# Kernel tuning notes

Hardware: AMD Instinct MI355X
Metric: run time of the kernel (lower is better)

Reference implementation:

```python
import jax, jax.numpy as jnp
import numpy as np

NH, NKV, HD = 16, 4, 64  # num_heads, num_kv_heads, head_dim
ROPE_BASE = 10000.0


def setup_inputs() -> dict:
    key = jax.random.key(0)
    ks = jax.random.split(key, 5)
    B, S, D = 2, 2048, 1024
    x = jax.random.normal(ks[0], (B, S, D), dtype=jnp.float32)
    # torch Linear layout: [out_features, in_features], xavier-ish scale
    Wq = jax.random.normal(ks[1], (NH * HD, D), dtype=jnp.float32) * 0.02
    Wk = jax.random.normal(ks[2], (NKV * HD, D), dtype=jnp.float32) * 0.02
    Wv = jax.random.normal(ks[3], (NKV * HD, D), dtype=jnp.float32) * 0.02
    Wo = jax.random.normal(ks[4], (D, NH * HD), dtype=jnp.float32) * 0.02
    return {"x": x, "Wq": Wq, "Wk": Wk, "Wv": Wv, "Wo": Wo}


def _rotate_half(t):
    t1, t2 = jnp.split(t, 2, axis=-1)
    return jnp.concatenate([-t2, t1], axis=-1)


def _rope_cos_sin(seq_len, dtype):
    inv_freq = 1.0 / (ROPE_BASE ** (jnp.arange(0, HD, 2, dtype=jnp.float32) / HD))
    freqs = jnp.outer(jnp.arange(seq_len, dtype=jnp.float32), inv_freq)  # [S, HD/2]
    emb = jnp.concatenate([freqs, freqs], axis=-1)                       # [S, HD]
    return jnp.cos(emb).astype(dtype), jnp.sin(emb).astype(dtype)


def reference(x, Wq, Wk, Wv, Wo):
    B, S, D = x.shape
    scale = 1.0 / np.sqrt(HD)
    # projections (torch Linear: y = x @ W.T)
    q = jnp.einsum('bsd,ed->bse', x, Wq).reshape(B, S, NH, HD).transpose(0, 2, 1, 3)
    k = jnp.einsum('bsd,ed->bse', x, Wk).reshape(B, S, NKV, HD).transpose(0, 2, 1, 3)
    v = jnp.einsum('bsd,ed->bse', x, Wv).reshape(B, S, NKV, HD).transpose(0, 2, 1, 3)
    # RoPE
    cos, sin = _rope_cos_sin(S, x.dtype)
    cos = cos[None, None]  # [1,1,S,HD]
    sin = sin[None, None]
    q = q * cos + _rotate_half(q) * sin
    k = k * cos + _rotate_half(k) * sin
    # GQA: repeat kv heads (matches expand+reshape: head h = kvh*rep + r)
    rep = NH // NKV
    k = jnp.repeat(k, rep, axis=1)  # [B,NH,S,HD]
    v = jnp.repeat(v, rep, axis=1)
    # scaled dot-product attention, causal
    scores = jnp.einsum('bhqd,bhkd->bhqk', q, k) * scale
    causal = jnp.triu(jnp.ones((S, S), dtype=bool), k=1)
    scores = jnp.where(causal, jnp.float32(-jnp.inf), scores)
    attn = jax.nn.softmax(scores.astype(jnp.float32), axis=-1).astype(q.dtype)
    out = jnp.einsum('bhqk,bhkd->bhqd', attn, v)
    out = out.transpose(0, 2, 1, 3).reshape(B, S, NH * HD)
    return jnp.einsum('bse,de->bsd', out, Wo)
```

## Files before the change

### kernel.cpp

```cpp
#include <hip/hip_runtime.h>
#include <hip/hip_bf16.h>
#include <math.h>

#define B_    2
#define S_    2048
#define D_    1024
#define NH_   16
#define NKV_  4
#define HD_   64
#define NTOK  (B_ * S_)
#define QKVN  (NH_ * HD_ + 2 * NKV_ * HD_)
#define REP   (NH_ / NKV_)

#define LOG2E 1.4426950408889634f

typedef __attribute__((ext_vector_type(8))) short short8;
typedef __attribute__((ext_vector_type(4))) float f32x4;

__device__ short  g_xb[(size_t)NTOK * D_];
__device__ short  g_wqkv[(size_t)QKVN * D_];
__device__ short  g_wob[(size_t)D_ * NH_ * HD_];
__device__ float  g_rc[(size_t)S_ * 32];
__device__ float  g_rs[(size_t)S_ * 32];
__device__ short  g_qb[(size_t)B_ * NH_  * S_ * HD_];
__device__ short  g_kb[(size_t)B_ * NKV_ * S_ * HD_];
__device__ short  g_vt[(size_t)B_ * NKV_ * HD_ * S_];
__device__ short  g_ao[(size_t)NTOK * NH_ * HD_];

static __device__ inline short f2bf(float f) {
  __hip_bfloat16 h = __float2bfloat16(f);
  return *reinterpret_cast<short*>(&h);
}
static __device__ inline unsigned pack2(float lo, float hi) {
  return ((unsigned)(unsigned short)f2bf(hi) << 16) | (unsigned)(unsigned short)f2bf(lo);
}

#define NX4   (NTOK * D_ / 4)
#define NWQ4  (NH_ * HD_ * D_ / 4)
#define NWK4  (NKV_ * HD_ * D_ / 4)
#define NWV4  NWK4
#define NWO4  (D_ * NH_ * HD_ / 4)
#define NCVT  (NX4 + NWQ4 + NWK4 + NWV4 + NWO4)

__global__ __launch_bounds__(256) void convert_all(const float* __restrict__ x,
                                                   const float* __restrict__ wq,
                                                   const float* __restrict__ wk,
                                                   const float* __restrict__ wv,
                                                   const float* __restrict__ wo) {
  int i = blockIdx.x * blockDim.x + threadIdx.x;
  if (i >= NCVT) return;
  const float* src; short* dst; int off;
  if (i < NX4)                          { src = x;  dst = g_xb;   off = i; }
  else if (i < NX4 + NWQ4)              { src = wq; dst = g_wqkv; off = i - NX4; }
  else if (i < NX4 + NWQ4 + NWK4)       { src = wk; dst = g_wqkv + (size_t)NWQ4 * 4;          off = i - NX4 - NWQ4; }
  else if (i < NX4 + NWQ4 + NWK4 + NWV4){ src = wv; dst = g_wqkv + (size_t)(NWQ4 + NWK4) * 4; off = i - NX4 - NWQ4 - NWK4; }
  else                                  { src = wo; dst = g_wob;  off = i - NX4 - NWQ4 - NWK4 - NWV4; }
  float4 v = ((const float4*)src)[off];
  short4 s;
  s.x = f2bf(v.x); s.y = f2bf(v.y); s.z = f2bf(v.z); s.w = f2bf(v.w);
  ((short4*)dst)[off] = s;
}

__global__ __launch_bounds__(256) void rope_tbl() {
  int i = blockIdx.x * blockDim.x + threadIdx.x;
  if (i >= S_ * 32) return;
  const int d = i & 31, s = i >> 5;
  const float inv = exp2f((float)d * (-13.287712379549449f / 32.0f));
  const float ang = (float)s * inv;
  float sn, cs;
  sincosf(ang, &sn, &cs);
  g_rc[i] = cs; g_rs[i] = sn;
}

__global__ __launch_bounds__(256) void gemm_qkv_rope() {
  const int w = threadIdx.x >> 6, lane = threadIdx.x & 63;
  const int m0 = blockIdx.x * 128 + w * 32;
  const int nb = blockIdx.y;
  const int n0 = nb * 64;
  const int lr = lane & 15, lk = (lane >> 4) * 8;

  f32x4 acc[2][4] = {};
  for (int k0 = 0; k0 < D_; k0 += 32) {
    short8 a0 = *(const short8*)(g_xb + (size_t)(m0 + lr) * D_ + k0 + lk);
    short8 a1 = *(const short8*)(g_xb + (size_t)(m0 + 16 + lr) * D_ + k0 + lk);
#pragma unroll
    for (int bj = 0; bj < 4; ++bj) {
      short8 bf = *(const short8*)(g_wqkv + (size_t)(n0 + bj * 16 + lr) * D_ + k0 + lk);
      acc[0][bj] = __builtin_amdgcn_mfma_f32_16x16x32_bf16(a0, bf, acc[0][bj], 0, 0, 0);
      acc[1][bj] = __builtin_amdgcn_mfma_f32_16x16x32_bf16(a1, bf, acc[1][bj], 0, 0, 0);
    }
  }
  const int rb = (lane >> 4) * 4;

  if (nb < 20) {
    const float sc = (nb < 16) ? 0.125f * LOG2E : 1.0f;
    short* const base = (nb < 16) ? g_qb : g_kb;
    const int hh = (nb < 16) ? nb : (nb - 16);
    const int nhh = (nb < 16) ? NH_ : NKV_;
#pragma unroll
    for (int af = 0; af < 2; ++af)
#pragma unroll
      for (int bj = 0; bj < 2; ++bj) {
        const int d0 = bj * 16 + lr;
#pragma unroll
        for (int r = 0; r < 4; ++r) {
          const int tok = m0 + af * 16 + rb + r;
          const int bI = tok >> 11, s = tok & (S_ - 1);
          const float c  = g_rc[s * 32 + d0];
          const float sn = g_rs[s * 32 + d0];
          const float lo = acc[af][bj][r], hi = acc[af][bj + 2][r];
          short* dp = base + (((size_t)(bI * nhh + hh)) * S_ + s) * HD_;
          dp[d0]      = f2bf((lo * c - hi * sn) * sc);
          dp[d0 + 32] = f2bf((hi * c + lo * sn) * sc);
        }
      }
  } else {
    const int kvh = nb - 20;
#pragma unroll
    for (int af = 0; af < 2; ++af)
#pragma unroll
      for (int bj = 0; bj < 4; ++bj) {
        const int d = bj * 16 + lr;
        const int tok0 = m0 + af * 16 + rb;
        const int bI = tok0 >> 11, s0 = tok0 & (S_ - 1);
        short4 s4;
        s4.x = f2bf(acc[af][bj][0]); s4.y = f2bf(acc[af][bj][1]);
        s4.z = f2bf(acc[af][bj][2]); s4.w = f2bf(acc[af][bj][3]);
        *(short4*)(g_vt + (((size_t)(bI * NKV_ + kvh)) * HD_ + d) * S_ + s0) = s4;
      }
  }
}

__global__ __launch_bounds__(64) void attn_mfma() {
  const int bh  = blockIdx.x;
  const int b   = bh >> 4, h = bh & 15;
  const int kvh = h >> 2;
  const int qw  = (int)(gridDim.y - 1 - blockIdx.y);
  const int lane = threadIdx.x;
  const int g = lane >> 4, l = lane & 15;
  const int q0 = qw * 16;
  const int q_glob = q0 + l;

  const short* Qb = g_qb + ((size_t)bh * S_ + q0) * HD_;
  const short* Kb = g_kb + ((size_t)(b * NKV_ + kvh)) * S_ * HD_;
  const short* Vt = g_vt + ((size_t)(b * NKV_ + kvh)) * HD_ * S_;

  short8 qf[2];
  qf[0] = *(const short8*)(Qb + l * HD_ + g * 8);
  qf[1] = *(const short8*)(Qb + l * HD_ + 32 + g * 8);

  f32x4 o[4] = {};
  float m_run = -1e30f, l_part = 0.0f;

  const int nt = (q0 >> 5) + 1;
  for (int t = 0; t < nt; ++t) {
    const short* Kt = Kb + (size_t)(t * 32) * HD_;
    short8 kf0 = *(const short8*)(Kt + l * HD_ + g * 8);
    short8 kf1 = *(const short8*)(Kt + (16 + l) * HD_ + g * 8);
    short8 kf2 = *(const short8*)(Kt + l * HD_ + 32 + g * 8);
    short8 kf3 = *(const short8*)(Kt + (16 + l) * HD_ + 32 + g * 8);
    short8 vf[4];
#pragma unroll
    for (int df = 0; df < 4; ++df)
      vf[df] = *(const short8*)(Vt + (size_t)(df * 16 + l) * S_ + t * 32 + g * 8);

    f32x4 st[2] = {};
    st[0] = __builtin_amdgcn_mfma_f32_16x16x32_bf16(kf0, qf[0], st[0], 0, 0, 0);
    st[1] = __builtin_amdgcn_mfma_f32_16x16x32_bf16(kf1, qf[0], st[1], 0, 0, 0);
    st[0] = __builtin_amdgcn_mfma_f32_16x16x32_bf16(kf2, qf[1], st[0], 0, 0, 0);
    st[1] = __builtin_amdgcn_mfma_f32_16x16x32_bf16(kf3, qf[1], st[1], 0, 0, 0);

    float sv[2][4];
    float mt = -1e30f;
#pragma unroll
    for (int mf = 0; mf < 2; ++mf)
#pragma unroll
      for (int r = 0; r < 4; ++r) {
        const int kv = t * 32 + mf * 16 + g * 4 + r;
        float s = st[mf][r];
        s = (kv > q_glob) ? -1e30f : s;
        sv[mf][r] = s;
        mt = fmaxf(mt, s);
      }
    if (__any(mt > m_run + 8.0f)) {
      float mr = mt;
      mr = fmaxf(mr, __shfl_xor(mr, 16, 64));
      mr = fmaxf(mr, __shfl_xor(mr, 32, 64));
      const float m_new = fmaxf(m_run, mr);
      const float alpha = exp2f(m_run - m_new);
      l_part *= alpha;
#pragma unroll
      for (int df = 0; df < 4; ++df)
#pragma unroll
        for (int r = 0; r < 4; ++r) o[df][r] *= alpha;
      m_run = m_new;
    }
    float p[2][4];
#pragma unroll
    for (int mf = 0; mf < 2; ++mf)
#pragma unroll
      for (int r = 0; r < 4; ++r) {
        const float pv = exp2f(sv[mf][r] - m_run);
        p[mf][r] = pv;
        l_part += pv;
      }
    unsigned u0 = pack2(p[0][0], p[0][1]);
    unsigned u1 = pack2(p[0][2], p[0][3]);
    unsigned u2 = pack2(p[1][0], p[1][1]);
    unsigned u3 = pack2(p[1][2], p[1][3]);
    const int srcA = ((g & 1) << 5) + l;
    const int srcB = srcA + 16;
    const unsigned a0 = __shfl(u0, srcA, 64), a2 = __shfl(u2, srcA, 64);
    const unsigned b1 = __shfl(u1, srcA, 64), b3 = __shfl(u3, srcA, 64);
    const unsigned c0 = __shfl(u0, srcB, 64), c2 = __shfl(u2, srcB, 64);
    const unsigned d1 = __shfl(u1, srcB, 64), d3 = __shfl(u3, srcB, 64);
    const bool hi = (g & 2);
    unsigned W[4];
    W[0] = hi ? a2 : a0;  W[1] = hi ? b3 : b1;
    W[2] = hi ? c2 : c0;  W[3] = hi ? d3 : d1;
    short8 pt = *reinterpret_cast<short8*>(W);

#pragma unroll
    for (int df = 0; df < 4; ++df)
      o[df] = __builtin_amdgcn_mfma_f32_16x16x32_bf16(vf[df], pt, o[df], 0, 0, 0);
  }

  float l1 = l_part + __shfl_xor(l_part, 16, 64);
  const float l_tot = l1 + __shfl_xor(l1, 32, 64);
  const float inv_l = 1.0f / l_tot;

  short* optr = g_ao + ((size_t)(b * S_ + q_glob)) * (NH_ * HD_) + h * HD_;
#pragma unroll
  for (int df = 0; df < 4; ++df) {
    short4 s4;
    s4.x = f2bf(o[df][0] * inv_l);
    s4.y = f2bf(o[df][1] * inv_l);
    s4.z = f2bf(o[df][2] * inv_l);
    s4.w = f2bf(o[df][3] * inv_l);
    *(short4*)(optr + df * 16 + g * 4) = s4;
  }
}

__global__ __launch_bounds__(256) void gemm_out(float* __restrict__ out) {
  const int w = threadIdx.x >> 6, lane = threadIdx.x & 63;
  const int m0 = blockIdx.x * 128 + w * 32;
  const int n0 = blockIdx.y * 64;
  const int lr = lane & 15, lk = (lane >> 4) * 8;
  const int K = NH_ * HD_;

  f32x4 acc[2][4] = {};
  for (int k0 = 0; k0 < K; k0 += 32) {
    short8 a0 = *(const short8*)(g_ao + (size_t)(m0 + lr) * K + k0 + lk);
    short8 a1 = *(const short8*)(g_ao + (size_t)(m0 + 16 + lr) * K + k0 + lk);
#pragma unroll
    for (int bj = 0; bj < 4; ++bj) {
      short8 bf = *(const short8*)(g_wob + (size_t)(n0 + bj * 16 + lr) * K + k0 + lk);
      acc[0][bj] = __builtin_amdgcn_mfma_f32_16x16x32_bf16(a0, bf, acc[0][bj], 0, 0, 0);
      acc[1][bj] = __builtin_amdgcn_mfma_f32_16x16x32_bf16(a1, bf, acc[1][bj], 0, 0, 0);
    }
  }
  const int rb = (lane >> 4) * 4;
#pragma unroll
  for (int af = 0; af < 2; ++af)
#pragma unroll
    for (int bj = 0; bj < 4; ++bj)
#pragma unroll
      for (int r = 0; r < 4; ++r)
        out[(size_t)(m0 + af * 16 + rb + r) * D_ + n0 + bj * 16 + lr] =
            acc[af][bj][r];
}

extern "C" void kernel_launch(void* const* d_in, const int* in_sizes, int n_in,
                              void* d_out, int out_size, void* d_ws, size_t ws_size,
                              hipStream_t stream) {
  const float* x  = (const float*)d_in[0];
  const float* Wq = (const float*)d_in[1];
  const float* Wk = (const float*)d_in[2];
  const float* Wv = (const float*)d_in[3];
  const float* Wo = (const float*)d_in[4];
  float* out = (float*)d_out;

  convert_all<<<(NCVT + 255) / 256, 256, 0, stream>>>(x, Wq, Wk, Wv, Wo);
  rope_tbl<<<(S_ * 32 + 255) / 256, 256, 0, stream>>>();
  {
    dim3 g(NTOK / 128, QKVN / 64);
    gemm_qkv_rope<<<g, 256, 0, stream>>>();
  }
  {
    dim3 g(B_ * NH_, S_ / 16);
    attn_mfma<<<g, 64, 0, stream>>>();
  }
  {
    dim3 g(NTOK / 128, D_ / 64);
    gemm_out<<<g, 256, 0, stream>>>(out);
  }
}
```

Before: 327.1 us.

## Split attention key tiles across four waves and merge partial softmax in LDS

The attention kernel grows from one wave to four waves per 16-query block. Each wave processes every fourth 32-key tile and keeps its own running max, sum and output accumulator. The four partial results are then combined through shared memory using a log-sum-exp rescale before the bf16 output is written. This shortens the long serial per-block loop over key tiles and hides more memory latency. In exchange it adds LDS traffic, a barrier and merge arithmetic, and leaves some waves idle on short causal rows.

```diff
diff --git a/kernel.cpp b/kernel.cpp
--- a/kernel.cpp
+++ b/kernel.cpp
@@ -131,12 +131,13 @@
   }
 }
 
-__global__ __launch_bounds__(64) void attn_mfma() {
+__global__ __launch_bounds__(256) void attn_mfma() {
   const int bh  = blockIdx.x;
   const int b   = bh >> 4, h = bh & 15;
   const int kvh = h >> 2;
   const int qw  = (int)(gridDim.y - 1 - blockIdx.y);
-  const int lane = threadIdx.x;
+  const int w   = threadIdx.x >> 6;
+  const int lane = threadIdx.x & 63;
   const int g = lane >> 4, l = lane & 15;
   const int q0 = qw * 16;
   const int q_glob = q0 + l;
@@ -153,7 +154,7 @@
   float m_run = -1e30f, l_part = 0.0f;
 
   const int nt = (q0 >> 5) + 1;
-  for (int t = 0; t < nt; ++t) {
+  for (int t = w; t < nt; t += 4) {
     const short* Kt = Kb + (size_t)(t * 32) * HD_;
     short8 kf0 = *(const short8*)(Kt + l * HD_ + g * 8);
     short8 kf1 = *(const short8*)(Kt + (16 + l) * HD_ + g * 8);
@@ -227,18 +228,40 @@
 
   float l1 = l_part + __shfl_xor(l_part, 16, 64);
   const float l_tot = l1 + __shfl_xor(l1, 32, 64);
-  const float inv_l = 1.0f / l_tot;
-
-  short* optr = g_ao + ((size_t)(b * S_ + q_glob)) * (NH_ * HD_) + h * HD_;
-#pragma unroll
-  for (int df = 0; df < 4; ++df) {
-    short4 s4;
-    s4.x = f2bf(o[df][0] * inv_l);
-    s4.y = f2bf(o[df][1] * inv_l);
-    s4.z = f2bf(o[df][2] * inv_l);
-    s4.w = f2bf(o[df][3] * inv_l);
-    *(short4*)(optr + df * 16 + g * 4) = s4;
-  }
+
+  __shared__ float lds_m[4][16];
+  __shared__ float lds_l[4][16];
+  __shared__ float lds_o[4][16][68];
+  if (g == 0) { lds_m[w][l] = m_run; lds_l[w][l] = l_tot; }
+#pragma unroll
+  for (int df = 0; df < 4; ++df)
+#pragma unroll
+    for (int r = 0; r < 4; ++r)
+      lds_o[w][l][df * 16 + g * 4 + r] = o[df][r];
+  __syncthreads();
+
+  const int tid = threadIdx.x;
+  const int q = tid & 15, dg = tid >> 4;
+  float ms = lds_m[0][q];
+#pragma unroll
+  for (int w2 = 1; w2 < 4; ++w2) ms = fmaxf(ms, lds_m[w2][q]);
+  float lsum = 0.0f;
+  float od[4] = {0.0f, 0.0f, 0.0f, 0.0f};
+#pragma unroll
+  for (int w2 = 0; w2 < 4; ++w2) {
+    const float sc = exp2f(lds_m[w2][q] - ms);
+    lsum += lds_l[w2][q] * sc;
+#pragma unroll
+    for (int j = 0; j < 4; ++j) od[j] += sc * lds_o[w2][q][dg * 4 + j];
+  }
+  const float inv_l = 1.0f / lsum;
+  short* optr = g_ao + ((size_t)(b * S_ + q0 + q)) * (NH_ * HD_) + h * HD_;
+  short4 s4;
+  s4.x = f2bf(od[0] * inv_l);
+  s4.y = f2bf(od[1] * inv_l);
+  s4.z = f2bf(od[2] * inv_l);
+  s4.w = f2bf(od[3] * inv_l);
+  *(short4*)(optr + dg * 4) = s4;
 }
 
 __global__ __launch_bounds__(256) void gemm_out(float* __restrict__ out) {
@@ -288,7 +311,7 @@
   }
   {
     dim3 g(B_ * NH_, S_ / 16);
-    attn_mfma<<<g, 64, 0, stream>>>();
+    attn_mfma<<<g, 256, 0, stream>>>();
   }
   {
     dim3 g(NTOK / 128, D_ / 64);
```

Result: no change. 322.9 us (-1.3%).
